# Kernel optimization log

Measured on AMD Instinct MI355X. Metric: run time of the kernel, lower is better.

Reference implementation:

```python
import jax, jax.numpy as jnp
import numpy as np

BLOCK_SIZE = 64
R_BLOCKS = 64          # r: number of rotation blocks (r * block_size == in_features)
N_ELEMENTS = BLOCK_SIZE * (BLOCK_SIZE - 1) // 2  # 2016
NUM_NEUMANN_TERMS = 5

# strict upper-triangular indices (matches torch.triu_indices(b, b, 1))
_ROWS, _COLS = np.triu_indices(BLOCK_SIZE, 1)


def _cayley_neumann(weight):
    """weight: (r, n_elements) -> batch of orthogonal-ish blocks (r, b, b)."""
    b = BLOCK_SIZE
    M = jnp.zeros((weight.shape[0], b, b), dtype=weight.dtype)
    M = M.at[:, _ROWS, _COLS].set(weight)
    Q = M - jnp.swapaxes(M, -1, -2)           # skew-symmetric (r, b, b)
    I = jnp.eye(b, dtype=weight.dtype)
    # R = I + 2Q + 2Q^2 + ... + 2Q^(terms-1)
    R = I + 2.0 * Q
    Qp = jnp.matmul(Q, Q)
    R = R + 2.0 * Qp
    for _ in range(3, NUM_NEUMANN_TERMS):
        Qp = jnp.matmul(Qp, Q)
        R = R + 2.0 * Qp
    return R


def setup_inputs() -> dict:
    key = jax.random.key(0)
    k_x, k_w = jax.random.split(key)
    x = jax.random.normal(k_x, (8192, 4096), dtype=jnp.float32)
    # small weights so the Neumann series approximates the Cayley transform
    weight = jax.random.normal(k_w, (R_BLOCKS, N_ELEMENTS), dtype=jnp.float32) * 0.01
    return {"x": x, "weight": weight}


def reference(x, weight):
    # x: (N, in_features); block-diagonal rotation applied per 64-wide block
    orth = _cayley_neumann(weight)                      # (r, b, b)
    N = x.shape[0]
    xr = x.reshape(N, R_BLOCKS, BLOCK_SIZE)             # (N, r, b)
    out = jnp.einsum("nrk,rkc->nrc", xr, orth)          # block-diag matmul
    return out.reshape(x.shape)
```

## Files before the change

### kernel.cpp

```cpp
#include <hip/hip_runtime.h>


#define LDP 68

typedef __attribute__((ext_vector_type(8))) short short8;
typedef __attribute__((ext_vector_type(4))) float f32x4;

static __device__ __forceinline__ unsigned short f2bf(float f) {
  unsigned u = __float_as_uint(f);
  u += 0x7FFF + ((u >> 16) & 1);
  return (unsigned short)(u >> 16);
}

__device__ __forceinline__ void mm_tile_68(const float (*A)[LDP], const float (*Bm)[LDP],
                                           int r0, int c0, float p[4][4]) {
  for (int k = 0; k < 64; k += 4) {
    float4 bv[4], av[4];
#pragma unroll
    for (int u = 0; u < 4; ++u) bv[u] = *(const float4*)&Bm[k + u][c0];
#pragma unroll
    for (int i = 0; i < 4; ++i) av[i] = *(const float4*)&A[r0 + i][k];
#pragma unroll
    for (int u = 0; u < 4; ++u) {
      const float4 b = bv[u];
#pragma unroll
      for (int i = 0; i < 4; ++i) {
        const float a = ((const float*)&av[i])[u];
        p[i][0] += a * b.x;
        p[i][1] += a * b.y;
        p[i][2] += a * b.z;
        p[i][3] += a * b.w;
      }
    }
  }
}


__global__ __launch_bounds__(256) void oft_build_R(const float* __restrict__ w,
                                                   unsigned* __restrict__ RT) {
  const int r = blockIdx.x;
  const int t = threadIdx.x;
  __shared__ float Q[64][LDP];
  __shared__ float P[64][LDP];
  __shared__ float T[64][LDP];

  for (int f = t; f < 64 * LDP; f += 256) (&Q[0][0])[f] = 0.f;
  __syncthreads();

  for (int i = t; i < 2016; i += 256) {
    int row = 0, rem = i;
    while (rem >= 63 - row) { rem -= 63 - row; ++row; }
    const int col = row + 1 + rem;
    const float v = w[r * 2016 + i];
    Q[row][col] = v;
    Q[col][row] = -v;
  }
  __syncthreads();

  const int r0 = (t >> 4) * 4, c0 = (t & 15) * 4;

  float p[4][4] = {};
  mm_tile_68(Q, Q, r0, c0, p);
#pragma unroll
  for (int i = 0; i < 4; ++i)
#pragma unroll
    for (int j = 0; j < 4; ++j) {
      P[r0 + i][c0 + j] = p[i][j];
      T[r0 + i][c0 + j] = p[i][j] + Q[r0 + i][c0 + j] + ((r0 + i) == (c0 + j) ? 1.f : 0.f);
    }
  __syncthreads();

  float p2[4][4] = {};
  mm_tile_68(P, T, r0, c0, p2);
  float acc[4][4];
#pragma unroll
  for (int i = 0; i < 4; ++i)
#pragma unroll
    for (int j = 0; j < 4; ++j)
      acc[i][j] = ((r0 + i) == (c0 + j) ? 1.f : 0.f)
                + 2.f * Q[r0 + i][c0 + j] + 2.f * p2[i][j];
  __syncthreads();

#pragma unroll
  for (int i = 0; i < 4; ++i)
#pragma unroll
    for (int j = 0; j < 4; ++j)
      T[c0 + j][r0 + i] = acc[i][j];
  __syncthreads();

#pragma unroll
  for (int i2 = 0; i2 < 8; ++i2) {
    const int f = t + 256 * i2;
    const int row = f >> 5, col = (f & 31) * 2;
    unsigned lo = f2bf(T[row][col]);
    unsigned hi = f2bf(T[row][col + 1]);
    RT[(size_t)r * 2048 + f] = lo | (hi << 16);
  }
}


__global__ __launch_bounds__(256) void oft_apply(const float* __restrict__ x,
                                                 const unsigned* __restrict__ RT,
                                                 float* __restrict__ out) {
  const int r = blockIdx.x;
  const int n0 = blockIdx.y * 128;
  const int t = threadIdx.x;

  __shared__ __align__(16) unsigned short Xs[128][72];
  __shared__ __align__(16) unsigned short Rs[64][72];

  {
    const uint4* Rg = (const uint4*)(RT + (size_t)r * 2048);
    uint4 v0 = Rg[t];
    uint4 v1 = Rg[t + 256];
    *(uint4*)&Rs[t >> 3][(t & 7) * 8] = v0;
    *(uint4*)&Rs[(t + 256) >> 3][((t + 256) & 7) * 8] = v1;
  }

#pragma unroll
  for (int i = 0; i < 8; ++i) {
    const int f = t + 256 * i;
    const int row = f >> 4, c4 = (f & 15) * 4;
    float4 v = *(const float4*)&x[(size_t)(n0 + row) * 4096 + r * 64 + c4];
    ushort4 b;
    b.x = f2bf(v.x); b.y = f2bf(v.y); b.z = f2bf(v.z); b.w = f2bf(v.w);
    *(ushort4*)&Xs[row][c4] = b;
  }
  __syncthreads();

  const int lane = t & 63, w = t >> 6;
  const int lo = lane & 15, q = lane >> 4;

  short8 bfr[2][4];
#pragma unroll
  for (int h = 0; h < 2; ++h)
#pragma unroll
    for (int c = 0; c < 4; ++c)
      bfr[h][c] = *(const short8*)&Rs[c * 16 + lo][h * 32 + q * 8];

  f32x4 acc[2][4];
#pragma unroll
  for (int s2 = 0; s2 < 2; ++s2)
#pragma unroll
    for (int c = 0; c < 4; ++c)
#pragma unroll
      for (int i = 0; i < 4; ++i) acc[s2][c][i] = 0.f;

#pragma unroll
  for (int s2 = 0; s2 < 2; ++s2) {
    const int s = w + 4 * s2;
#pragma unroll
    for (int h = 0; h < 2; ++h) {
      short8 a = *(const short8*)&Xs[s * 16 + lo][h * 32 + q * 8];
#pragma unroll
      for (int c = 0; c < 4; ++c)
        acc[s2][c] = __builtin_amdgcn_mfma_f32_16x16x32_bf16(a, bfr[h][c], acc[s2][c], 0, 0, 0);
    }
  }

#pragma unroll
  for (int s2 = 0; s2 < 2; ++s2) {
    const int s = w + 4 * s2;
#pragma unroll
    for (int c = 0; c < 4; ++c)
#pragma unroll
      for (int i = 0; i < 4; ++i) {
        const int row = n0 + s * 16 + q * 4 + i;
        out[(size_t)row * 4096 + r * 64 + c * 16 + lo] = acc[s2][c][i];
      }
  }
}

extern "C" void kernel_launch(void* const* d_in, const int* in_sizes, int n_in,
                              void* d_out, int out_size, void* d_ws, size_t ws_size,
                              hipStream_t stream) {
  const float* x = (const float*)d_in[0];
  const float* w = (const float*)d_in[1];
  float* out = (float*)d_out;
  unsigned* RTws = (unsigned*)d_ws;

  oft_build_R<<<64, 256, 0, stream>>>(w, RTws);
  oft_apply<<<dim3(64, 64), 256, 0, stream>>>(x, RTws, out);
}
```

Baseline: 250.4 us.

## Load x directly into MFMA registers with prefetch and nontemporal stores

Result: slower. 261.8 us (+4.5%).

```diff
diff --git a/kernel.cpp b/kernel.cpp
--- a/kernel.cpp
+++ b/kernel.cpp
@@ -10,6 +10,15 @@
   unsigned u = __float_as_uint(f);
   u += 0x7FFF + ((u >> 16) & 1);
   return (unsigned short)(u >> 16);
+}
+
+static __device__ __forceinline__ short8 pack8(float4 a, float4 b) {
+  short8 s;
+  s[0] = (short)f2bf(a.x); s[1] = (short)f2bf(a.y);
+  s[2] = (short)f2bf(a.z); s[3] = (short)f2bf(a.w);
+  s[4] = (short)f2bf(b.x); s[5] = (short)f2bf(b.y);
+  s[6] = (short)f2bf(b.z); s[7] = (short)f2bf(b.w);
+  return s;
 }
 
 __device__ __forceinline__ void mm_tile_68(const float (*A)[LDP], const float (*Bm)[LDP],
@@ -99,32 +108,22 @@
 }
 
 
+#define WAVES 4
+#define TILES 4
+
 __global__ __launch_bounds__(256) void oft_apply(const float* __restrict__ x,
                                                  const unsigned* __restrict__ RT,
                                                  float* __restrict__ out) {
   const int r = blockIdx.x;
-  const int n0 = blockIdx.y * 128;
   const int t = threadIdx.x;
 
-  __shared__ __align__(16) unsigned short Xs[128][72];
   __shared__ __align__(16) unsigned short Rs[64][72];
-
   {
     const uint4* Rg = (const uint4*)(RT + (size_t)r * 2048);
     uint4 v0 = Rg[t];
     uint4 v1 = Rg[t + 256];
     *(uint4*)&Rs[t >> 3][(t & 7) * 8] = v0;
     *(uint4*)&Rs[(t + 256) >> 3][((t + 256) & 7) * 8] = v1;
-  }
-
-#pragma unroll
-  for (int i = 0; i < 8; ++i) {
-    const int f = t + 256 * i;
-    const int row = f >> 4, c4 = (f & 15) * 4;
-    float4 v = *(const float4*)&x[(size_t)(n0 + row) * 4096 + r * 64 + c4];
-    ushort4 b;
-    b.x = f2bf(v.x); b.y = f2bf(v.y); b.z = f2bf(v.z); b.w = f2bf(v.w);
-    *(ushort4*)&Xs[row][c4] = b;
   }
   __syncthreads();
 
@@ -138,36 +137,47 @@
     for (int c = 0; c < 4; ++c)
       bfr[h][c] = *(const short8*)&Rs[c * 16 + lo][h * 32 + q * 8];
 
-  f32x4 acc[2][4];
+  const size_t colOff = (size_t)r * 64;
+  const int rowBase = blockIdx.y * (WAVES * TILES * 16);
+  const size_t tileStride = (size_t)(WAVES * 16) * 4096;
+
+  const float* lp = x + (size_t)(rowBase + w * 16 + lo) * 4096 + colOff + (size_t)q * 8;
+  float* sp = out + (size_t)(rowBase + w * 16 + q * 4) * 4096 + colOff + lo;
+
+  float4 L0 = *(const float4*)(lp + 0);
+  float4 L1 = *(const float4*)(lp + 4);
+  float4 L2 = *(const float4*)(lp + 32);
+  float4 L3 = *(const float4*)(lp + 36);
+
 #pragma unroll
-  for (int s2 = 0; s2 < 2; ++s2)
+  for (int tt = 0; tt < TILES; ++tt) {
+    float4 C0 = L0, C1 = L1, C2 = L2, C3 = L3;
+    if (tt + 1 < TILES) {
+      const float* np = lp + (size_t)(tt + 1) * tileStride;
+      L0 = *(const float4*)(np + 0);
+      L1 = *(const float4*)(np + 4);
+      L2 = *(const float4*)(np + 32);
+      L3 = *(const float4*)(np + 36);
+    }
+    short8 a0 = pack8(C0, C1);
+    short8 a1 = pack8(C2, C3);
+
+    f32x4 acc[4];
+#pragma unroll
+    for (int c = 0; c < 4; ++c) { acc[c][0] = 0.f; acc[c][1] = 0.f; acc[c][2] = 0.f; acc[c][3] = 0.f; }
+#pragma unroll
+    for (int c = 0; c < 4; ++c)
+      acc[c] = __builtin_amdgcn_mfma_f32_16x16x32_bf16(a0, bfr[0][c], acc[c], 0, 0, 0);
+#pragma unroll
+    for (int c = 0; c < 4; ++c)
+      acc[c] = __builtin_amdgcn_mfma_f32_16x16x32_bf16(a1, bfr[1][c], acc[c], 0, 0, 0);
+
+    float* op = sp + (size_t)tt * tileStride;
 #pragma unroll
     for (int c = 0; c < 4; ++c)
 #pragma unroll
-      for (int i = 0; i < 4; ++i) acc[s2][c][i] = 0.f;
-
-#pragma unroll
-  for (int s2 = 0; s2 < 2; ++s2) {
-    const int s = w + 4 * s2;
-#pragma unroll
-    for (int h = 0; h < 2; ++h) {
-      short8 a = *(const short8*)&Xs[s * 16 + lo][h * 32 + q * 8];
-#pragma unroll
-      for (int c = 0; c < 4; ++c)
-        acc[s2][c] = __builtin_amdgcn_mfma_f32_16x16x32_bf16(a, bfr[h][c], acc[s2][c], 0, 0, 0);
-    }
-  }
-
-#pragma unroll
-  for (int s2 = 0; s2 < 2; ++s2) {
-    const int s = w + 4 * s2;
-#pragma unroll
-    for (int c = 0; c < 4; ++c)
-#pragma unroll
-      for (int i = 0; i < 4; ++i) {
-        const int row = n0 + s * 16 + q * 4 + i;
-        out[(size_t)row * 4096 + r * 64 + c * 16 + lo] = acc[s2][c][i];
-      }
+      for (int i = 0; i < 4; ++i)
+        __builtin_nontemporal_store(acc[c][i], op + (size_t)i * 4096 + c * 16);
   }
 }
 
@@ -180,5 +190,5 @@
   unsigned* RTws = (unsigned*)d_ws;
 
   oft_build_R<<<64, 256, 0, stream>>>(w, RTws);
-  oft_apply<<<dim3(64, 64), 256, 0, stream>>>(x, RTws, out);
+  oft_apply<<<dim3(64, 8192 / (WAVES * TILES * 16)), 256, 0, stream>>>(x, RTws, out);
 }
```
